# Optimization experiments

Hardware: AMD Instinct MI355X
Metric: run time of the kernel (lower is better)

Reference implementation:

```python
import jax, jax.numpy as jnp
import numpy as np
from jax import lax

INP = 512
OUT = 512
T = 2048
B = 64


def setup_inputs() -> dict:
    key = jax.random.key(0)
    ks = jax.random.split(key, 7)
    rang = (1.0 / OUT) ** 0.5
    u = lambda k, shape: jax.random.uniform(k, shape, jnp.float32, -rang, rang)
    return {
        "x": jax.random.normal(ks[0], (T, B, INP), jnp.float32),
        "g": u(ks[1], (INP, OUT)),
        "gb": u(ks[2], (OUT,)),
        "h": u(ks[3], (INP, OUT)),
        "hb": u(ks[4], (OUT,)),
        "r": u(ks[5], (1, OUT)),
        "rb": u(ks[6], (OUT,)),
    }


def reference(x, g, gb, h, hb, r, rb):
    # x: [T, B, inp]
    Tn = x.shape[0]
    # time gate: r_t = 2*sigmoid((n/T) * r + rb), shape [T, out]
    t = (jnp.arange(Tn, dtype=x.dtype) / Tn)[:, None]  # [T, 1]
    rt = 2.0 * jax.nn.sigmoid(t * r[0] + rb)           # [T, out]
    # precompute per-step gates (vectorized over T)
    G = jax.nn.sigmoid(jnp.einsum("tbi,io->tbo", x, g) + gb) * rt[:, None, :]
    H = jnp.tanh(jnp.einsum("tbi,io->tbo", x, h) + hb) * rt[:, None, :]

    def step(y, gh):
        g_t, h_t = gh
        return y * g_t + h_t, None

    y0 = jnp.zeros((x.shape[1], x.shape[2] * 0 + G.shape[-1]), dtype=x.dtype)
    y, _ = lax.scan(step, y0, (G, H))
    return y
```

## Files before the change

### kernel.cpp

```cpp
#include <hip/hip_runtime.h>
#include <cstdint>
#include <cstddef>

#define TT   2048
#define BB   64
#define KK   512
#define OO   512
#define NCH  64
#define TC   32

typedef __attribute__((ext_vector_type(8))) short short8;
typedef __attribute__((ext_vector_type(4))) float f32x4;

__device__ __forceinline__ unsigned short f2bf(float f) {
  unsigned int u = __float_as_uint(f);
  unsigned int rounding = 0x7FFFu + ((u >> 16) & 1u);
  return (unsigned short)((u + rounding) >> 16);
}

__device__ __forceinline__ float sigmoid_f(float z) {
  return 1.0f / (1.0f + __expf(-z));
}

__device__ __forceinline__ float tanh_f(float z) {
  z = fminf(15.0f, fmaxf(-15.0f, z));
  float e = __expf(-2.0f * z);
  return (1.0f - e) / (1.0f + e);
}

__device__ __forceinline__ void async_ld16(const void* g, void* l) {
  __builtin_amdgcn_global_load_lds(
      (const __attribute__((address_space(1))) void*)g,
      (__attribute__((address_space(3))) void*)l, 16, 0, 0);
}

__global__ void convert_x_k(const float4* __restrict__ x4,
                            ushort4* __restrict__ xb4, int n4) {
  int i = blockIdx.x * blockDim.x + threadIdx.x;
  int stride = gridDim.x * blockDim.x;
  for (; i < n4; i += stride) {
    float4 v = x4[i];
    ushort4 o;
    o.x = f2bf(v.x); o.y = f2bf(v.y); o.z = f2bf(v.z); o.w = f2bf(v.w);
    xb4[i] = o;
  }
}

__global__ void prep_weights_k(const float* __restrict__ g,
                               const float* __restrict__ h,
                               unsigned short* __restrict__ Gt,
                               unsigned short* __restrict__ Ht) {
  __shared__ float tile[32][33];
  const float* src = (blockIdx.z == 0) ? g : h;
  unsigned short* dst = (blockIdx.z == 0) ? Gt : Ht;
  int ox = blockIdx.x * 32;
  int ky = blockIdx.y * 32;
  int tx = threadIdx.x, ty = threadIdx.y;
  #pragma unroll
  for (int r = ty; r < 32; r += 8)
    tile[r][tx] = src[(ky + r) * OO + ox + tx];
  __syncthreads();
  #pragma unroll
  for (int r = ty; r < 32; r += 8)
    dst[(size_t)(ox + r) * KK + ky + tx] = f2bf(tile[tx][r]);
}

__global__ __launch_bounds__(512, 2) void rnn_fused4_k(
    const unsigned short* __restrict__ xb,
    const unsigned short* __restrict__ Gt,
    const unsigned short* __restrict__ Ht,
    const float* __restrict__ gb, const float* __restrict__ hb,
    const float* __restrict__ r,  const float* __restrict__ rb,
    float* __restrict__ chunkA, float* __restrict__ chunkB) {
  extern __shared__ __align__(16) unsigned short smem[];

  const int tid  = threadIdx.x;
  const int wave = tid >> 6;
  const int lane = tid & 63;
  const int quad = lane >> 4;
  const int lcol = lane & 15;

  const int bi = blockIdx.x;
  const int ot = bi >> 6;
  const int c  = bi & 63;
  const int o  = ot * 128 + wave * 16 + lcol;

  const float gbv = gb[o], hbv = hb[o];
  const float rv  = r[o],  rbv = rb[o];

  short8 Bg[16], Bh[16];
  {
    const unsigned short* gp = Gt + (size_t)o * KK + quad * 8;
    const unsigned short* hp = Ht + (size_t)o * KK + quad * 8;
    #pragma unroll
    for (int K16 = 0; K16 < 16; ++K16) {
      Bg[K16] = *(const short8*)(gp + K16 * 32);
      Bh[K16] = *(const short8*)(hp + K16 * 32);
    }
  }

  auto stage = [&](int s) {
    unsigned short* dst = smem + (s & 3) * 16384 + wave * 2048;
    const int t = c * TC + (s >> 1);
    const unsigned short* srcb = xb + (size_t)t * (BB * KK) + (s & 1) * 256;
    #pragma unroll
    for (int j = 0; j < 4; ++j) {
      int rr  = 2 * j + (lane >> 5);
      int gch = (lane & 31) ^ rr;
      async_ld16(srcb + (size_t)(wave * 8 + rr) * KK + gch * 8,
                 dst + j * 512);
    }
  };

  stage(0); stage(1); stage(2);

  float SA[16], SB[16];
  #pragma unroll
  for (int s2 = 0; s2 < 16; ++s2) { SA[s2] = 1.0f; SB[s2] = 0.0f; }

  f32x4 accG[4], accH[4];
  #pragma unroll
  for (int m = 0; m < 4; m++) {
    f32x4 z = {0.0f, 0.0f, 0.0f, 0.0f};
    accG[m] = z; accH[m] = z;
  }

  for (int t = 0; t < TC; ++t) {
    const int b0 = (t & 1) * 2;
    #pragma unroll
    for (int h = 0; h < 2; ++h) {
      if (t < TC - 1) {
        asm volatile("s_waitcnt vmcnt(8)" ::: "memory");
      } else if (h == 0) {
        asm volatile("s_waitcnt vmcnt(4)" ::: "memory");
      } else {
        asm volatile("s_waitcnt vmcnt(0)" ::: "memory");
      }
      __builtin_amdgcn_sched_barrier(0);
      __builtin_amdgcn_s_barrier();

      const int sn = 2 * t + h + 3;
      if (sn < 2 * TC) stage(sn);

      const unsigned short* A0 = smem + (b0 + h) * 16384;
      __builtin_amdgcn_s_setprio(1);
      #pragma unroll
      for (int k2 = 0; k2 < 8; ++k2) {
        const int K16 = h * 8 + k2;
        #pragma unroll
        for (int mt = 0; mt < 4; ++mt) {
          const int arow = mt * 16 + lcol;
          const int sl   = (k2 * 4 + quad) ^ (lcol & 7);
          short8 a = *(const short8*)(A0 + arow * 256 + sl * 8);
          accG[mt] = __builtin_amdgcn_mfma_f32_16x16x32_bf16(
              a, Bg[K16], accG[mt], 0, 0, 0);
          accH[mt] = __builtin_amdgcn_mfma_f32_16x16x32_bf16(
              a, Bh[K16], accH[mt], 0, 0, 0);
        }
      }
      __builtin_amdgcn_s_setprio(0);
    }

    const int tt = c * TC + t;
    const float rt = 2.0f * sigmoid_f(((float)tt * (1.0f / TT)) * rv + rbv);
    #pragma unroll
    for (int mt = 0; mt < 4; ++mt)
      #pragma unroll
      for (int reg = 0; reg < 4; ++reg) {
        float G = sigmoid_f(accG[mt][reg] + gbv) * rt;
        float H = tanh_f  (accH[mt][reg] + hbv) * rt;
        int s2 = mt * 4 + reg;
        SB[s2] = fmaf(G, SB[s2], H);
        SA[s2] *= G;
        accG[mt][reg] = 0.0f;
        accH[mt][reg] = 0.0f;
      }
  }

  #pragma unroll
  for (int mt = 0; mt < 4; ++mt)
    #pragma unroll
    for (int reg = 0; reg < 4; ++reg) {
      int s2 = mt * 4 + reg;
      int b = mt * 16 + quad * 4 + reg;
      size_t idx = ((size_t)c * BB + b) * OO + o;
      chunkA[idx] = SA[s2];
      chunkB[idx] = SB[s2];
    }
}

__global__ void combine_k(const float* __restrict__ cA,
                          const float* __restrict__ cB,
                          float* __restrict__ out) {
  int i = blockIdx.x * blockDim.x + threadIdx.x;
  float y = 0.0f;
  #pragma unroll 8
  for (int c = 0; c < NCH; c++) {
    float A  = cA[(size_t)c * (BB * OO) + i];
    float Bv = cB[(size_t)c * (BB * OO) + i];
    y = fmaf(A, y, Bv);
  }
  out[i] = y;
}

extern "C" void kernel_launch(void* const* d_in, const int* in_sizes, int n_in,
                              void* d_out, int out_size, void* d_ws, size_t ws_size,
                              hipStream_t stream) {
  (void)in_sizes; (void)n_in; (void)out_size; (void)ws_size;
  const float* x  = (const float*)d_in[0];
  const float* g  = (const float*)d_in[1];
  const float* gb = (const float*)d_in[2];
  const float* h  = (const float*)d_in[3];
  const float* hb = (const float*)d_in[4];
  const float* r  = (const float*)d_in[5];
  const float* rb = (const float*)d_in[6];
  float* out = (float*)d_out;

  char* w = (char*)d_ws;
  unsigned short* xb = (unsigned short*)w;
  unsigned short* Gt = (unsigned short*)(w + 134217728);
  unsigned short* Ht = (unsigned short*)(w + 134742016);
  float* chunkA = (float*)(w + 135266304);
  float* chunkB = (float*)(w + 143654912);

  static bool attr_set = false;
  if (!attr_set) {
    hipFuncSetAttribute(reinterpret_cast<const void*>(rnn_fused4_k),
                        hipFuncAttributeMaxDynamicSharedMemorySize, 131072);
    attr_set = true;
  }

  const int n4 = (TT * BB * KK) / 4;
  convert_x_k<<<8192, 256, 0, stream>>>((const float4*)x, (ushort4*)xb, n4);
  prep_weights_k<<<dim3(16, 16, 2), dim3(32, 8), 0, stream>>>(g, h, Gt, Ht);
  rnn_fused4_k<<<NCH * 4, 512, 131072, stream>>>(xb, Gt, Ht, gb, hb, r, rb,
                                                 chunkA, chunkB);
  combine_k<<<(BB * OO) / 256, 256, 0, stream>>>(chunkA, chunkB, out);
}
```

Measured before the change: 541.9 us.

## Halve waves per block, give each wave two output column tiles, use rcp activations

The fused RNN kernel now runs 4 waves per block instead of 8. Each wave covers 32 output columns (two 16-wide tiles), so every LDS A-fragment load feeds four MFMAs instead of two. Each wave stages twice as many rows, and the LDS swizzle pattern changes to match. Sigmoid and tanh now use the hardware reciprocal approximation, and the s_setprio hints are dropped. In exchange, register pressure roughly doubles (weights, accumulators and scan state), and each block has fewer waves to hide latency.

```diff
diff --git a/kernel.cpp b/kernel.cpp
--- a/kernel.cpp
+++ b/kernel.cpp
@@ -18,14 +18,11 @@
   return (unsigned short)((u + rounding) >> 16);
 }
 
-__device__ __forceinline__ float sigmoid_f(float z) {
-  return 1.0f / (1.0f + __expf(-z));
-}
-
-__device__ __forceinline__ float tanh_f(float z) {
-  z = fminf(15.0f, fmaxf(-15.0f, z));
-  float e = __expf(-2.0f * z);
-  return (1.0f - e) / (1.0f + e);
+__device__ __forceinline__ float fast_sigmoid(float z) {
+  return __builtin_amdgcn_rcpf(1.0f + __expf(-z));
+}
+__device__ __forceinline__ float fast_tanh(float z) {
+  return fmaf(2.0f, __builtin_amdgcn_rcpf(1.0f + __expf(-2.0f * z)), -1.0f);
 }
 
 __device__ __forceinline__ void async_ld16(const void* g, void* l) {
@@ -65,7 +62,7 @@
     dst[(size_t)(ox + r) * KK + ky + tx] = f2bf(tile[tx][r]);
 }
 
-__global__ __launch_bounds__(512, 2) void rnn_fused4_k(
+__global__ __launch_bounds__(256, 1) void rnn_fused5_k(
     const unsigned short* __restrict__ xb,
     const unsigned short* __restrict__ Gt,
     const unsigned short* __restrict__ Ht,
@@ -83,110 +80,123 @@
   const int bi = blockIdx.x;
   const int ot = bi >> 6;
   const int c  = bi & 63;
-  const int o  = ot * 128 + wave * 16 + lcol;
-
-  const float gbv = gb[o], hbv = hb[o];
-  const float rv  = r[o],  rbv = rb[o];
-
-  short8 Bg[16], Bh[16];
-  {
-    const unsigned short* gp = Gt + (size_t)o * KK + quad * 8;
-    const unsigned short* hp = Ht + (size_t)o * KK + quad * 8;
+  const int o0 = ot * 128 + wave * 32 + lcol;
+
+  float gbv[2], hbv[2], rv[2], rbv[2];
+  #pragma unroll
+  for (int cb = 0; cb < 2; ++cb) {
+    int o = o0 + cb * 16;
+    gbv[cb] = gb[o]; hbv[cb] = hb[o];
+    rv[cb]  = r[o];  rbv[cb] = rb[o];
+  }
+
+  short8 Bg[2][16], Bh[2][16];
+  #pragma unroll
+  for (int cb = 0; cb < 2; ++cb) {
+    const unsigned short* gp = Gt + (size_t)(o0 + cb * 16) * KK + quad * 8;
+    const unsigned short* hp = Ht + (size_t)(o0 + cb * 16) * KK + quad * 8;
     #pragma unroll
     for (int K16 = 0; K16 < 16; ++K16) {
-      Bg[K16] = *(const short8*)(gp + K16 * 32);
-      Bh[K16] = *(const short8*)(hp + K16 * 32);
+      Bg[cb][K16] = *(const short8*)(gp + K16 * 32);
+      Bh[cb][K16] = *(const short8*)(hp + K16 * 32);
     }
   }
 
   auto stage = [&](int s) {
-    unsigned short* dst = smem + (s & 3) * 16384 + wave * 2048;
+    unsigned short* dst = smem + (s & 3) * 16384 + wave * 4096;
     const int t = c * TC + (s >> 1);
     const unsigned short* srcb = xb + (size_t)t * (BB * KK) + (s & 1) * 256;
     #pragma unroll
-    for (int j = 0; j < 4; ++j) {
-      int rr  = 2 * j + (lane >> 5);
-      int gch = (lane & 31) ^ rr;
-      async_ld16(srcb + (size_t)(wave * 8 + rr) * KK + gch * 8,
-                 dst + j * 512);
+    for (int j = 0; j < 8; ++j) {
+      int rr  = wave * 16 + 2 * j + (lane >> 5);
+      int gch = (lane & 31) ^ ((rr & 7) << 2);
+      async_ld16(srcb + (size_t)rr * KK + gch * 8, dst + j * 512);
     }
   };
 
   stage(0); stage(1); stage(2);
 
-  float SA[16], SB[16];
-  #pragma unroll
-  for (int s2 = 0; s2 < 16; ++s2) { SA[s2] = 1.0f; SB[s2] = 0.0f; }
-
-  f32x4 accG[4], accH[4];
-  #pragma unroll
-  for (int m = 0; m < 4; m++) {
-    f32x4 z = {0.0f, 0.0f, 0.0f, 0.0f};
-    accG[m] = z; accH[m] = z;
-  }
+  float SA[32], SB[32];
+  #pragma unroll
+  for (int s2 = 0; s2 < 32; ++s2) { SA[s2] = 1.0f; SB[s2] = 0.0f; }
+
+  f32x4 accG[2][4], accH[2][4];
+  #pragma unroll
+  for (int cb = 0; cb < 2; ++cb)
+    #pragma unroll
+    for (int m = 0; m < 4; ++m) {
+      f32x4 z = {0.0f, 0.0f, 0.0f, 0.0f};
+      accG[cb][m] = z; accH[cb][m] = z;
+    }
 
   for (int t = 0; t < TC; ++t) {
-    const int b0 = (t & 1) * 2;
     #pragma unroll
     for (int h = 0; h < 2; ++h) {
       if (t < TC - 1) {
+        asm volatile("s_waitcnt vmcnt(16)" ::: "memory");
+      } else if (h == 0) {
         asm volatile("s_waitcnt vmcnt(8)" ::: "memory");
-      } else if (h == 0) {
-        asm volatile("s_waitcnt vmcnt(4)" ::: "memory");
       } else {
         asm volatile("s_waitcnt vmcnt(0)" ::: "memory");
       }
       __builtin_amdgcn_sched_barrier(0);
       __builtin_amdgcn_s_barrier();
-
-      const int sn = 2 * t + h + 3;
-      if (sn < 2 * TC) stage(sn);
-
-      const unsigned short* A0 = smem + (b0 + h) * 16384;
-      __builtin_amdgcn_s_setprio(1);
+      __builtin_amdgcn_sched_barrier(0);
+
+      const int s = 2 * t + h;
+      if (s + 3 < 2 * TC) stage(s + 3);
+
+      const unsigned short* A0 = smem + (s & 3) * 16384;
       #pragma unroll
       for (int k2 = 0; k2 < 8; ++k2) {
-        const int K16 = h * 8 + k2;
         #pragma unroll
         for (int mt = 0; mt < 4; ++mt) {
           const int arow = mt * 16 + lcol;
-          const int sl   = (k2 * 4 + quad) ^ (lcol & 7);
+          const int sl   = (k2 * 4 + quad) ^ ((lcol & 7) << 2);
           short8 a = *(const short8*)(A0 + arow * 256 + sl * 8);
-          accG[mt] = __builtin_amdgcn_mfma_f32_16x16x32_bf16(
-              a, Bg[K16], accG[mt], 0, 0, 0);
-          accH[mt] = __builtin_amdgcn_mfma_f32_16x16x32_bf16(
-              a, Bh[K16], accH[mt], 0, 0, 0);
+          #pragma unroll
+          for (int cb = 0; cb < 2; ++cb) {
+            accG[cb][mt] = __builtin_amdgcn_mfma_f32_16x16x32_bf16(
+                a, Bg[cb][h * 8 + k2], accG[cb][mt], 0, 0, 0);
+            accH[cb][mt] = __builtin_amdgcn_mfma_f32_16x16x32_bf16(
+                a, Bh[cb][h * 8 + k2], accH[cb][mt], 0, 0, 0);
+          }
         }
       }
-      __builtin_amdgcn_s_setprio(0);
     }
 
     const int tt = c * TC + t;
-    const float rt = 2.0f * sigmoid_f(((float)tt * (1.0f / TT)) * rv + rbv);
+    const float tn = (float)tt * (1.0f / TT);
+    #pragma unroll
+    for (int cb = 0; cb < 2; ++cb) {
+      const float rt = 2.0f * fast_sigmoid(tn * rv[cb] + rbv[cb]);
+      #pragma unroll
+      for (int mt = 0; mt < 4; ++mt)
+        #pragma unroll
+        for (int reg = 0; reg < 4; ++reg) {
+          float G = fast_sigmoid(accG[cb][mt][reg] + gbv[cb]) * rt;
+          float H = fast_tanh  (accH[cb][mt][reg] + hbv[cb]) * rt;
+          int s2 = cb * 16 + mt * 4 + reg;
+          SB[s2] = fmaf(G, SB[s2], H);
+          SA[s2] *= G;
+          accG[cb][mt][reg] = 0.0f;
+          accH[cb][mt][reg] = 0.0f;
+        }
+    }
+  }
+
+  #pragma unroll
+  for (int cb = 0; cb < 2; ++cb)
     #pragma unroll
     for (int mt = 0; mt < 4; ++mt)
       #pragma unroll
       for (int reg = 0; reg < 4; ++reg) {
-        float G = sigmoid_f(accG[mt][reg] + gbv) * rt;
-        float H = tanh_f  (accH[mt][reg] + hbv) * rt;
-        int s2 = mt * 4 + reg;
-        SB[s2] = fmaf(G, SB[s2], H);
-        SA[s2] *= G;
-        accG[mt][reg] = 0.0f;
-        accH[mt][reg] = 0.0f;
+        int s2 = cb * 16 + mt * 4 + reg;
+        int b = mt * 16 + quad * 4 + reg;
+        size_t idx = ((size_t)c * BB + b) * OO + (o0 + cb * 16);
+        chunkA[idx] = SA[s2];
+        chunkB[idx] = SB[s2];
       }
-  }
-
-  #pragma unroll
-  for (int mt = 0; mt < 4; ++mt)
-    #pragma unroll
-    for (int reg = 0; reg < 4; ++reg) {
-      int s2 = mt * 4 + reg;
-      int b = mt * 16 + quad * 4 + reg;
-      size_t idx = ((size_t)c * BB + b) * OO + o;
-      chunkA[idx] = SA[s2];
-      chunkB[idx] = SB[s2];
-    }
 }
 
 __global__ void combine_k(const float* __restrict__ cA,
@@ -225,7 +235,7 @@
 
   static bool attr_set = false;
   if (!attr_set) {
-    hipFuncSetAttribute(reinterpret_cast<const void*>(rnn_fused4_k),
+    hipFuncSetAttribute(reinterpret_cast<const void*>(rnn_fused5_k),
                         hipFuncAttributeMaxDynamicSharedMemorySize, 131072);
     attr_set = true;
   }
@@ -233,7 +243,7 @@
   const int n4 = (TT * BB * KK) / 4;
   convert_x_k<<<8192, 256, 0, stream>>>((const float4*)x, (ushort4*)xb, n4);
   prep_weights_k<<<dim3(16, 16, 2), dim3(32, 8), 0, stream>>>(g, h, Gt, Ht);
-  rnn_fused4_k<<<NCH * 4, 512, 131072, stream>>>(xb, Gt, Ht, gb, hb, r, rb,
+  rnn_fused5_k<<<NCH * 4, 256, 131072, stream>>>(xb, Gt, Ht, gb, hb, r, rb,
                                                  chunkA, chunkB);
   combine_k<<<(BB * OO) / 256, 256, 0, stream>>>(chunkA, chunkB, out);
 }
```

Result: slower. 557.7 us (+2.9%).
